# Kernel tuning notes

Measured on AMD Instinct MI355X. Metric: run time of the kernel, lower is better.

The kernel has to match this reference:

```python
import jax, jax.numpy as jnp
import numpy as np

B, C, T, H, W, E, K = 2, 256, 16, 32, 32, 4, 2


def setup_inputs() -> dict:
    key = jax.random.key(0)
    ks = jax.random.split(key, 5)
    x = jax.random.normal(ks[0], (B, C, T, H, W), dtype=jnp.float32)
    # gate: Conv3d(dim, E, 1) -> weight [E, C], bias [E]
    gate_w = jax.random.normal(ks[1], (E, C), dtype=jnp.float32) * 0.02
    gate_b = jnp.zeros((E,), dtype=jnp.float32)
    # experts_layer1: Conv3d(dim, dim*E, 1) -> weight [E*C, C], bias [E*C]
    w1 = jax.random.normal(ks[2], (E * C, C), dtype=jnp.float32) * 0.02
    b1 = jnp.zeros((E * C,), dtype=jnp.float32)
    # experts_layer2: Conv3d(dim*E, dim*E, 1, groups=E) -> per-expert [C, C]
    w2 = jax.random.normal(ks[3], (E, C, C), dtype=jnp.float32) * 0.02
    b2 = jnp.zeros((E, C), dtype=jnp.float32)
    return {"x": x, "gate_w": gate_w, "gate_b": gate_b,
            "w1": w1, "b1": b1, "w2": w2, "b2": b2}


def reference(x, gate_w, gate_b, w1, b1, w2, b2):
    # gating: 1x1x1 conv == channel contraction; logits [B,T,H,W,E]
    logits = jnp.einsum('bcthw,ec->bthwe', x, gate_w) + gate_b
    vals, idx = jax.lax.top_k(logits, K)              # [B,T,H,W,K]
    wk = jax.nn.softmax(vals, axis=-1).astype(x.dtype)
    # scatter top-k softmax weights back into E slots (zeros elsewhere)
    weights = jnp.sum(jax.nn.one_hot(idx, E, dtype=x.dtype) * wk[..., None],
                      axis=-2)                        # [B,T,H,W,E]
    # layer1 (dense 1x1x1 conv) + SiLU; output channels = E*C
    h = jax.nn.silu(jnp.einsum('bcthw,oc->bothw', x, w1)
                    + b1[None, :, None, None, None])
    h = h.reshape(B, E, C, T, H, W)
    # layer2: grouped 1x1x1 conv, one [C,C] matmul per expert
    expert_out = (jnp.einsum('becthw,eoc->beothw', h, w2)
                  + b2[None, :, :, None, None, None])  # [B,E,C,T,H,W]
    # weighted combine over experts + residual
    out = jnp.einsum('becthw,bthwe->bcthw', expert_out, weights)
    return out + x
```

## Files before the change

### kernel.cpp

```cpp
#include <hip/hip_runtime.h>
#include <hip/hip_bf16.h>


#define C_DIM 256
#define S_DIM 16384
#define E_DIM 4
#define MT 64
#define XST 264
#define OST 68
#define WFRAG_ELEMS 262144

typedef __attribute__((ext_vector_type(8))) short bf16x8;
typedef __attribute__((ext_vector_type(4))) short short4v;
typedef __attribute__((ext_vector_type(4))) float f32x4;

__device__ __forceinline__ short bfq(float f) {
  __hip_bfloat16 h = __float2bfloat16(f);
  return *(short*)&h;
}

__global__ __launch_bounds__(256) void prepack_kernel(
    const float* __restrict__ w1, const float* __restrict__ w2,
    __hip_bfloat16* __restrict__ dst)
{
  int o = blockIdx.x * 256 + threadIdx.x;
  int half = o >> 18;
  int idx = o & (WFRAG_ELEMS - 1);
  int j    = idx & 7;
  int lane = (idx >> 3) & 63;
  int kc   = (idx >> 9) & 7;
  int nt   = (idx >> 12) & 15;
  int e    = (idx >> 16) & 3;
  const float* src = half ? w2 : w1;
  int si = (e*256 + nt*16 + (lane & 15))*256 + kc*32 + (lane >> 4)*8 + j;
  dst[o] = __float2bfloat16(src[si]);
}

__global__ __launch_bounds__(256, 2) void moe_fused_kernel(
    const float* __restrict__ x,
    const float* __restrict__ gate_w,
    const float* __restrict__ gate_b,
    const float* __restrict__ b1,
    const float* __restrict__ b2,
    const __hip_bfloat16* __restrict__ wp,
    float* __restrict__ out)
{
  __shared__ __align__(16) char pool[256 * OST * 4];
  __shared__ float Wgt[MT * 4];

  short* XsS = (short*)pool;
  short* HsS = (short*)(pool + MT * XST * 2);
  float* Os  = (float*)pool;

  const int tid  = threadIdx.x;
  const int lane = tid & 63;
  const int wv   = tid >> 6;
  const int r    = lane & 15;
  const int q    = lane >> 4;

  const int g  = blockIdx.x;
  const int b  = g >> 8;
  const int s0 = (g & 255) * MT;
  const float* xb = x + (size_t)b * C_DIM * S_DIM + s0;

  {
    const int p4 = (tid & 15) * 4;
    const int cg = tid >> 4;
#pragma unroll
    for (int cc = 0; cc < 4; ++cc) {
      const int c0 = (cc*16 + cg) * 4;
      const float4 v0 = *(const float4*)(xb + (size_t)(c0+0)*S_DIM + p4);
      const float4 v1 = *(const float4*)(xb + (size_t)(c0+1)*S_DIM + p4);
      const float4 v2 = *(const float4*)(xb + (size_t)(c0+2)*S_DIM + p4);
      const float4 v3 = *(const float4*)(xb + (size_t)(c0+3)*S_DIM + p4);
      *(short4v*)(XsS + (p4+0)*XST + c0) = (short4v){bfq(v0.x), bfq(v1.x), bfq(v2.x), bfq(v3.x)};
      *(short4v*)(XsS + (p4+1)*XST + c0) = (short4v){bfq(v0.y), bfq(v1.y), bfq(v2.y), bfq(v3.y)};
      *(short4v*)(XsS + (p4+2)*XST + c0) = (short4v){bfq(v0.z), bfq(v1.z), bfq(v2.z), bfq(v3.z)};
      *(short4v*)(XsS + (p4+3)*XST + c0) = (short4v){bfq(v0.w), bfq(v1.w), bfq(v2.w), bfq(v3.w)};
    }
  }

  {
    const int p = lane;
    const int e = wv;
    const float* gw = gate_w + e * C_DIM;
    const float* xr = xb + p;
    double a0 = 0.0, a1 = 0.0, a2 = 0.0, a3 = 0.0;
#pragma unroll 4
    for (int c = 0; c < C_DIM; c += 4) {
      a0 += (double)xr[(size_t)(c+0) * S_DIM] * (double)gw[c+0];
      a1 += (double)xr[(size_t)(c+1) * S_DIM] * (double)gw[c+1];
      a2 += (double)xr[(size_t)(c+2) * S_DIM] * (double)gw[c+2];
      a3 += (double)xr[(size_t)(c+3) * S_DIM] * (double)gw[c+3];
    }
    Wgt[p*4 + e] = (float)(((a0 + a1) + (a2 + a3)) + (double)gate_b[e]);
  }
  __syncthreads();

  if (tid < MT) {
    const int p = tid;
    const float l0 = Wgt[p*4+0], l1 = Wgt[p*4+1], l2 = Wgt[p*4+2], l3 = Wgt[p*4+3];
    int i1 = 0; float v1 = l0;
    if (l1 > v1) { v1 = l1; i1 = 1; }
    if (l2 > v1) { v1 = l2; i1 = 2; }
    if (l3 > v1) { v1 = l3; i1 = 3; }
    float v2 = -3.0e38f; int i2 = 0;
    if (i1 != 0 && l0 > v2) { v2 = l0; i2 = 0; }
    if (i1 != 1 && l1 > v2) { v2 = l1; i2 = 1; }
    if (i1 != 2 && l2 > v2) { v2 = l2; i2 = 2; }
    if (i1 != 3 && l3 > v2) { v2 = l3; i2 = 3; }
    const float wA = 1.0f / (1.0f + __expf(v2 - v1));
    const float wB = 1.0f - wA;
    Wgt[p*4+0] = (i1 == 0) ? wA : ((i2 == 0) ? wB : 0.0f);
    Wgt[p*4+1] = (i1 == 1) ? wA : ((i2 == 1) ? wB : 0.0f);
    Wgt[p*4+2] = (i1 == 2) ? wA : ((i2 == 2) ? wB : 0.0f);
    Wgt[p*4+3] = (i1 == 3) ? wA : ((i2 == 3) ? wB : 0.0f);
  }
  __syncthreads();

  const short* W1P = (const short*)wp;
  const short* W2P = (const short*)wp + WFRAG_ELEMS;

  f32x4 oacc[4][4];
#pragma unroll
  for (int i = 0; i < 4; ++i)
#pragma unroll
    for (int j = 0; j < 4; ++j) oacc[i][j] = (f32x4){0.f, 0.f, 0.f, 0.f};

  for (int e = 0; e < E_DIM; ++e) {
    f32x4 hacc[4][4];
#pragma unroll
    for (int i = 0; i < 4; ++i)
#pragma unroll
      for (int j = 0; j < 4; ++j) hacc[i][j] = (f32x4){0.f, 0.f, 0.f, 0.f};

    {
      const short* w1e = W1P + ((e*16 + wv*4)*8)*512 + lane*8;
      bf16x8 bw[3][4];
#pragma unroll
      for (int t = 0; t < 4; ++t) bw[0][t] = *(const bf16x8*)(w1e + (t*8 + 0)*512);
#pragma unroll
      for (int t = 0; t < 4; ++t) bw[1][t] = *(const bf16x8*)(w1e + (t*8 + 1)*512);
#pragma unroll
      for (int kc = 0; kc < 8; ++kc) {
        if (kc < 6) {
#pragma unroll
          for (int t = 0; t < 4; ++t)
            bw[(kc+2)%3][t] = *(const bf16x8*)(w1e + (t*8 + kc + 2)*512);
        }
        bf16x8 a[4];
#pragma unroll
        for (int Mt = 0; Mt < 4; ++Mt)
          a[Mt] = *(const bf16x8*)(XsS + (Mt*16 + r)*XST + kc*32 + q*8);
#pragma unroll
        for (int Mt = 0; Mt < 4; ++Mt)
#pragma unroll
          for (int t = 0; t < 4; ++t)
            hacc[Mt][t] = __builtin_amdgcn_mfma_f32_16x16x32_bf16(a[Mt], bw[kc%3][t], hacc[Mt][t], 0, 0, 0);
      }
    }

    const short* w2e = W2P + ((e*16 + wv*4)*8)*512 + lane*8;
    bf16x8 cw[3][4];
#pragma unroll
    for (int t = 0; t < 4; ++t) cw[0][t] = *(const bf16x8*)(w2e + (t*8 + 0)*512);
#pragma unroll
    for (int t = 0; t < 4; ++t) cw[1][t] = *(const bf16x8*)(w2e + (t*8 + 1)*512);

    {
      float wreg[4][4];
#pragma unroll
      for (int Mt = 0; Mt < 4; ++Mt)
#pragma unroll
        for (int reg = 0; reg < 4; ++reg)
          wreg[Mt][reg] = Wgt[(Mt*16 + q*4 + reg)*4 + e];
#pragma unroll
      for (int t = 0; t < 4; ++t) {
        const int n = wv*64 + t*16 + r;
        const float bias = b1[e*256 + n];
#pragma unroll
        for (int Mt = 0; Mt < 4; ++Mt)
#pragma unroll
          for (int reg = 0; reg < 4; ++reg) {
            const float z = hacc[Mt][t][reg] + bias;
            const float s = __builtin_amdgcn_rcpf(1.0f + __expf(-z));
            const float h = z * s * wreg[Mt][reg];
            HsS[(Mt*16 + q*4 + reg)*XST + n] = bfq(h);
          }
      }
    }
    __syncthreads();

    {
#pragma unroll
      for (int kc = 0; kc < 8; ++kc) {
        if (kc < 6) {
#pragma unroll
          for (int t = 0; t < 4; ++t)
            cw[(kc+2)%3][t] = *(const bf16x8*)(w2e + (t*8 + kc + 2)*512);
        }
        bf16x8 a[4];
#pragma unroll
        for (int Mt = 0; Mt < 4; ++Mt)
          a[Mt] = *(const bf16x8*)(HsS + (Mt*16 + r)*XST + kc*32 + q*8);
#pragma unroll
        for (int Mt = 0; Mt < 4; ++Mt)
#pragma unroll
          for (int t = 0; t < 4; ++t)
            oacc[Mt][t] = __builtin_amdgcn_mfma_f32_16x16x32_bf16(a[Mt], cw[kc%3][t], oacc[Mt][t], 0, 0, 0);
      }
    }
    __syncthreads();
  }

  {
    float b2v[4][4];
#pragma unroll
    for (int t = 0; t < 4; ++t) {
      const int c = wv*64 + t*16 + r;
#pragma unroll
      for (int e = 0; e < 4; ++e) b2v[t][e] = b2[e*256 + c];
    }
#pragma unroll
    for (int Mt = 0; Mt < 4; ++Mt) {
      f32x4 wv4[4];
#pragma unroll
      for (int reg = 0; reg < 4; ++reg)
        wv4[reg] = *(const f32x4*)(&Wgt[(Mt*16 + q*4 + reg)*4]);
#pragma unroll
      for (int t = 0; t < 4; ++t) {
        f32x4 v = oacc[Mt][t];
#pragma unroll
        for (int reg = 0; reg < 4; ++reg)
          v[reg] += wv4[reg][0]*b2v[t][0] + wv4[reg][1]*b2v[t][1]
                  + wv4[reg][2]*b2v[t][2] + wv4[reg][3]*b2v[t][3];
        *(f32x4*)(Os + (size_t)(wv*64 + t*16 + r)*OST + Mt*16 + q*4) = v;
      }
    }
  }
  __syncthreads();

  {
    const int p4 = (tid & 15) * 4;
    const int cg = tid >> 4;
    float* ob = out + (size_t)b * C_DIM * S_DIM + s0;
#pragma unroll
    for (int cc = 0; cc < 16; ++cc) {
      const int c = cc*16 + cg;
      const f32x4  o  = *(const f32x4*)(Os + (size_t)c*OST + p4);
      const float4 xr = *(const float4*)(xb + (size_t)c*S_DIM + p4);
      float4 res;
      res.x = o[0] + xr.x; res.y = o[1] + xr.y;
      res.z = o[2] + xr.z; res.w = o[3] + xr.w;
      *(float4*)(ob + (size_t)c*S_DIM + p4) = res;
    }
  }
}

extern "C" void kernel_launch(void* const* d_in, const int* in_sizes, int n_in,
                              void* d_out, int out_size, void* d_ws, size_t ws_size,
                              hipStream_t stream)
{
  (void)in_sizes; (void)n_in; (void)out_size; (void)ws_size;
  const float* x      = (const float*)d_in[0];
  const float* gate_w = (const float*)d_in[1];
  const float* gate_b = (const float*)d_in[2];
  const float* w1     = (const float*)d_in[3];
  const float* b1     = (const float*)d_in[4];
  const float* w2     = (const float*)d_in[5];
  const float* b2     = (const float*)d_in[6];
  float* out = (float*)d_out;
  __hip_bfloat16* wpack = (__hip_bfloat16*)d_ws;

  prepack_kernel<<<2048, 256, 0, stream>>>(w1, w2, wpack);
  moe_fused_kernel<<<512, 256, 0, stream>>>(x, gate_w, gate_b, b1, b2, wpack, out);
}
```

Baseline: 146.8 us.

## Double workgroup to 512 threads, halve per-wave N tile and split gate reduction

Each block now runs 8 waves instead of 4. Each wave covers 32 output channels instead of 64, so accumulator registers are halved and the weight prefetch buffer drops from triple to double buffering. The gate dot product is split across two channel halves with fp64 partial sums in a new shared array, and the partials are combined before top-k. The aim is more waves in flight per CU to hide latency, at the cost of reloading the LDS A fragments twice as often per MFMA and a shallower weight prefetch.

New measurement: 136.9 us. 6.7% less time.

```diff
diff --git a/kernel.cpp b/kernel.cpp
--- a/kernel.cpp
+++ b/kernel.cpp
@@ -36,7 +36,7 @@
   dst[o] = __float2bfloat16(src[si]);
 }
 
-__global__ __launch_bounds__(256, 2) void moe_fused_kernel(
+__global__ __launch_bounds__(512, 4) void moe_fused_kernel(
     const float* __restrict__ x,
     const float* __restrict__ gate_w,
     const float* __restrict__ gate_b,
@@ -47,6 +47,7 @@
 {
   __shared__ __align__(16) char pool[256 * OST * 4];
   __shared__ float Wgt[MT * 4];
+  __shared__ double GateP[512];
 
   short* XsS = (short*)pool;
   short* HsS = (short*)(pool + MT * XST * 2);
@@ -67,8 +68,8 @@
     const int p4 = (tid & 15) * 4;
     const int cg = tid >> 4;
 #pragma unroll
-    for (int cc = 0; cc < 4; ++cc) {
-      const int c0 = (cc*16 + cg) * 4;
+    for (int cc = 0; cc < 2; ++cc) {
+      const int c0 = (cc*32 + cg) * 4;
       const float4 v0 = *(const float4*)(xb + (size_t)(c0+0)*S_DIM + p4);
       const float4 v1 = *(const float4*)(xb + (size_t)(c0+1)*S_DIM + p4);
       const float4 v2 = *(const float4*)(xb + (size_t)(c0+2)*S_DIM + p4);
@@ -81,34 +82,38 @@
   }
 
   {
-    const int p = lane;
-    const int e = wv;
-    const float* gw = gate_w + e * C_DIM;
-    const float* xr = xb + p;
+    const int p  = lane;
+    const int e  = wv & 3;
+    const int ch = wv >> 2;
+    const float* gw = gate_w + e * C_DIM + ch * 128;
+    const float* xr = xb + p + (size_t)(ch * 128) * S_DIM;
     double a0 = 0.0, a1 = 0.0, a2 = 0.0, a3 = 0.0;
 #pragma unroll 4
-    for (int c = 0; c < C_DIM; c += 4) {
+    for (int c = 0; c < 128; c += 4) {
       a0 += (double)xr[(size_t)(c+0) * S_DIM] * (double)gw[c+0];
       a1 += (double)xr[(size_t)(c+1) * S_DIM] * (double)gw[c+1];
       a2 += (double)xr[(size_t)(c+2) * S_DIM] * (double)gw[c+2];
       a3 += (double)xr[(size_t)(c+3) * S_DIM] * (double)gw[c+3];
     }
-    Wgt[p*4 + e] = (float)(((a0 + a1) + (a2 + a3)) + (double)gate_b[e]);
+    GateP[(ch*64 + p)*4 + e] = (a0 + a1) + (a2 + a3);
   }
   __syncthreads();
 
   if (tid < MT) {
     const int p = tid;
-    const float l0 = Wgt[p*4+0], l1 = Wgt[p*4+1], l2 = Wgt[p*4+2], l3 = Wgt[p*4+3];
-    int i1 = 0; float v1 = l0;
-    if (l1 > v1) { v1 = l1; i1 = 1; }
-    if (l2 > v1) { v1 = l2; i1 = 2; }
-    if (l3 > v1) { v1 = l3; i1 = 3; }
+    float l[4];
+#pragma unroll
+    for (int e = 0; e < 4; ++e)
+      l[e] = (float)(GateP[p*4 + e] + GateP[(64 + p)*4 + e] + (double)gate_b[e]);
+    int i1 = 0; float v1 = l[0];
+    if (l[1] > v1) { v1 = l[1]; i1 = 1; }
+    if (l[2] > v1) { v1 = l[2]; i1 = 2; }
+    if (l[3] > v1) { v1 = l[3]; i1 = 3; }
     float v2 = -3.0e38f; int i2 = 0;
-    if (i1 != 0 && l0 > v2) { v2 = l0; i2 = 0; }
-    if (i1 != 1 && l1 > v2) { v2 = l1; i2 = 1; }
-    if (i1 != 2 && l2 > v2) { v2 = l2; i2 = 2; }
-    if (i1 != 3 && l3 > v2) { v2 = l3; i2 = 3; }
+    if (i1 != 0 && l[0] > v2) { v2 = l[0]; i2 = 0; }
+    if (i1 != 1 && l[1] > v2) { v2 = l[1]; i2 = 1; }
+    if (i1 != 2 && l[2] > v2) { v2 = l[2]; i2 = 2; }
+    if (i1 != 3 && l[3] > v2) { v2 = l[3]; i2 = 3; }
     const float wA = 1.0f / (1.0f + __expf(v2 - v1));
     const float wB = 1.0f - wA;
     Wgt[p*4+0] = (i1 == 0) ? wA : ((i2 == 0) ? wB : 0.0f);
@@ -121,32 +126,30 @@
   const short* W1P = (const short*)wp;
   const short* W2P = (const short*)wp + WFRAG_ELEMS;
 
-  f32x4 oacc[4][4];
+  f32x4 oacc[4][2];
 #pragma unroll
   for (int i = 0; i < 4; ++i)
 #pragma unroll
-    for (int j = 0; j < 4; ++j) oacc[i][j] = (f32x4){0.f, 0.f, 0.f, 0.f};
+    for (int j = 0; j < 2; ++j) oacc[i][j] = (f32x4){0.f, 0.f, 0.f, 0.f};
 
   for (int e = 0; e < E_DIM; ++e) {
-    f32x4 hacc[4][4];
+    f32x4 hacc[4][2];
 #pragma unroll
     for (int i = 0; i < 4; ++i)
 #pragma unroll
-      for (int j = 0; j < 4; ++j) hacc[i][j] = (f32x4){0.f, 0.f, 0.f, 0.f};
+      for (int j = 0; j < 2; ++j) hacc[i][j] = (f32x4){0.f, 0.f, 0.f, 0.f};
 
     {
-      const short* w1e = W1P + ((e*16 + wv*4)*8)*512 + lane*8;
-      bf16x8 bw[3][4];
-#pragma unroll
-      for (int t = 0; t < 4; ++t) bw[0][t] = *(const bf16x8*)(w1e + (t*8 + 0)*512);
-#pragma unroll
-      for (int t = 0; t < 4; ++t) bw[1][t] = *(const bf16x8*)(w1e + (t*8 + 1)*512);
+      const short* w1e = W1P + ((e*16 + wv*2)*8)*512 + lane*8;
+      bf16x8 bw[2][2];
+#pragma unroll
+      for (int t = 0; t < 2; ++t) bw[0][t] = *(const bf16x8*)(w1e + (t*8 + 0)*512);
 #pragma unroll
       for (int kc = 0; kc < 8; ++kc) {
-        if (kc < 6) {
-#pragma unroll
-          for (int t = 0; t < 4; ++t)
-            bw[(kc+2)%3][t] = *(const bf16x8*)(w1e + (t*8 + kc + 2)*512);
+        if (kc < 7) {
+#pragma unroll
+          for (int t = 0; t < 2; ++t)
+            bw[(kc+1)&1][t] = *(const bf16x8*)(w1e + (t*8 + kc + 1)*512);
         }
         bf16x8 a[4];
 #pragma unroll
@@ -155,17 +158,15 @@
 #pragma unroll
         for (int Mt = 0; Mt < 4; ++Mt)
 #pragma unroll
-          for (int t = 0; t < 4; ++t)
-            hacc[Mt][t] = __builtin_amdgcn_mfma_f32_16x16x32_bf16(a[Mt], bw[kc%3][t], hacc[Mt][t], 0, 0, 0);
-      }
-    }
-
-    const short* w2e = W2P + ((e*16 + wv*4)*8)*512 + lane*8;
-    bf16x8 cw[3][4];
-#pragma unroll
-    for (int t = 0; t < 4; ++t) cw[0][t] = *(const bf16x8*)(w2e + (t*8 + 0)*512);
-#pragma unroll
-    for (int t = 0; t < 4; ++t) cw[1][t] = *(const bf16x8*)(w2e + (t*8 + 1)*512);
+          for (int t = 0; t < 2; ++t)
+            hacc[Mt][t] = __builtin_amdgcn_mfma_f32_16x16x32_bf16(a[Mt], bw[kc&1][t], hacc[Mt][t], 0, 0, 0);
+      }
+    }
+
+    const short* w2e = W2P + ((e*16 + wv*2)*8)*512 + lane*8;
+    bf16x8 cw[2][2];
+#pragma unroll
+    for (int t = 0; t < 2; ++t) cw[0][t] = *(const bf16x8*)(w2e + (t*8 + 0)*512);
 
     {
       float wreg[4][4];
@@ -175,8 +176,8 @@
         for (int reg = 0; reg < 4; ++reg)
           wreg[Mt][reg] = Wgt[(Mt*16 + q*4 + reg)*4 + e];
 #pragma unroll
-      for (int t = 0; t < 4; ++t) {
-        const int n = wv*64 + t*16 + r;
+      for (int t = 0; t < 2; ++t) {
+        const int n = wv*32 + t*16 + r;
         const float bias = b1[e*256 + n];
 #pragma unroll
         for (int Mt = 0; Mt < 4; ++Mt)
@@ -194,10 +195,10 @@
     {
 #pragma unroll
       for (int kc = 0; kc < 8; ++kc) {
-        if (kc < 6) {
-#pragma unroll
-          for (int t = 0; t < 4; ++t)
-            cw[(kc+2)%3][t] = *(const bf16x8*)(w2e + (t*8 + kc + 2)*512);
+        if (kc < 7) {
+#pragma unroll
+          for (int t = 0; t < 2; ++t)
+            cw[(kc+1)&1][t] = *(const bf16x8*)(w2e + (t*8 + kc + 1)*512);
         }
         bf16x8 a[4];
 #pragma unroll
@@ -206,18 +207,18 @@
 #pragma unroll
         for (int Mt = 0; Mt < 4; ++Mt)
 #pragma unroll
-          for (int t = 0; t < 4; ++t)
-            oacc[Mt][t] = __builtin_amdgcn_mfma_f32_16x16x32_bf16(a[Mt], cw[kc%3][t], oacc[Mt][t], 0, 0, 0);
+          for (int t = 0; t < 2; ++t)
+            oacc[Mt][t] = __builtin_amdgcn_mfma_f32_16x16x32_bf16(a[Mt], cw[kc&1][t], oacc[Mt][t], 0, 0, 0);
       }
     }
     __syncthreads();
   }
 
   {
-    float b2v[4][4];
-#pragma unroll
-    for (int t = 0; t < 4; ++t) {
-      const int c = wv*64 + t*16 + r;
+    float b2v[2][4];
+#pragma unroll
+    for (int t = 0; t < 2; ++t) {
+      const int c = wv*32 + t*16 + r;
 #pragma unroll
       for (int e = 0; e < 4; ++e) b2v[t][e] = b2[e*256 + c];
     }
@@ -228,13 +229,13 @@
       for (int reg = 0; reg < 4; ++reg)
         wv4[reg] = *(const f32x4*)(&Wgt[(Mt*16 + q*4 + reg)*4]);
 #pragma unroll
-      for (int t = 0; t < 4; ++t) {
+      for (int t = 0; t < 2; ++t) {
         f32x4 v = oacc[Mt][t];
 #pragma unroll
         for (int reg = 0; reg < 4; ++reg)
           v[reg] += wv4[reg][0]*b2v[t][0] + wv4[reg][1]*b2v[t][1]
                   + wv4[reg][2]*b2v[t][2] + wv4[reg][3]*b2v[t][3];
-        *(f32x4*)(Os + (size_t)(wv*64 + t*16 + r)*OST + Mt*16 + q*4) = v;
+        *(f32x4*)(Os + (size_t)(wv*32 + t*16 + r)*OST + Mt*16 + q*4) = v;
       }
     }
   }
@@ -245,8 +246,8 @@
     const int cg = tid >> 4;
     float* ob = out + (size_t)b * C_DIM * S_DIM + s0;
 #pragma unroll
-    for (int cc = 0; cc < 16; ++cc) {
-      const int c = cc*16 + cg;
+    for (int cc = 0; cc < 8; ++cc) {
+      const int c = cc*32 + cg;
       const f32x4  o  = *(const f32x4*)(Os + (size_t)c*OST + p4);
       const float4 xr = *(const float4*)(xb + (size_t)c*S_DIM + p4);
       float4 res;
@@ -273,5 +274,5 @@
   __hip_bfloat16* wpack = (__hip_bfloat16*)d_ws;
 
   prepack_kernel<<<2048, 256, 0, stream>>>(w1, w2, wpack);
-  moe_fused_kernel<<<512, 256, 0, stream>>>(x, gate_w, gate_b, b1, b2, wpack, out);
-}
+  moe_fused_kernel<<<512, 512, 0, stream>>>(x, gate_w, gate_b, b1, b2, wpack, out);
+}
```
